# Performance work log

Measured on AMD Instinct MI355X. Metric: run time of the kernel, lower is better.

The kernel has to match this reference:

```python
import jax, jax.numpy as jnp
import numpy as np

T, B, F, H, O = 2048, 256, 64, 256, 1

def setup_inputs() -> dict:
    key = jax.random.key(0)
    k0, k1, k2 = jax.random.split(key, 3)
    return {
        "x": jax.random.normal(k0, (T, B, F), jnp.float32),          # (Time, Batch, Feat)
        "W0": jax.random.normal(k1, (H, F + H), jnp.float32) * 0.05,  # i2h weight (PyTorch layout)
        "b0": jnp.zeros((H,), jnp.float32),
        "Wfc": jax.random.normal(k2, (O, H), jnp.float32) * 0.05,     # fc1 weight
        "bfc": jnp.zeros((O,), jnp.float32),
        "feature_n": 0,
    }

def reference(x, W0, b0, Wfc, bfc, feature_n):
    # RnnCell: h = tanh(Linear(cat([x_t, h], 1))); then out_t = fc1(h).
    batch = x.shape[1]
    hidden = W0.shape[0]
    h0 = jnp.zeros((batch, hidden), x.dtype)

    def step(h, x_t):
        combined = jnp.concatenate([x_t, h], axis=1)          # (B, F+H)
        h_new = jnp.tanh(combined @ W0.T + b0)                # (B, H)
        out = h_new @ Wfc.T + bfc                             # (B, O)
        return h_new, out

    _, outs = jax.lax.scan(step, h0, x)                       # (T, B, O)
    # torch.stack(outputs, 1).squeeze(2) -> (B, T)
    return jnp.transpose(outs, (1, 0, 2)).squeeze(2)
```

## Files before the change

kernel.cpp:

```cpp
#include <hip/hip_runtime.h>

#define T_STEPS 2048
#define BATCH   256
#define FEAT    64
#define HID     256
#define KAUG    320
#define NW      4
#define NTHR    256
#define XTILE   16

typedef _Float16 half8 __attribute__((ext_vector_type(8)));
typedef _Float16 half4 __attribute__((ext_vector_type(4)));
typedef float    f32x4 __attribute__((ext_vector_type(4)));
typedef float    f32x8 __attribute__((ext_vector_type(8)));

__device__ __forceinline__ float fast_tanh(float z) {
    float e = __expf(2.0f * z);
    return 1.0f - 2.0f * __builtin_amdgcn_rcpf(e + 1.0f);
}

__global__
__attribute__((amdgpu_flat_work_group_size(NTHR, NTHR), amdgpu_waves_per_eu(1, 1)))
void rnn_kernel(const float* __restrict__ x,
                const float* __restrict__ W0,
                const float* __restrict__ b0,
                const float* __restrict__ Wfc,
                const float* __restrict__ bfc,
                float* __restrict__ out)
{
    const int b    = blockIdx.x;
    const int tid  = threadIdx.x;
    const int w    = tid >> 6;
    const int lane = tid & 63;
    const int l15  = lane & 15;
    const int kg   = lane >> 4;
    const bool alane = (l15 == 0);

    __shared__ __align__(16) _Float16 h_buf[2][HID];
    __shared__ __align__(16) _Float16 x_tile[2][XTILE][FEAT];
    __shared__ __align__(16) float    out_part[NW][T_STEPS];

    half8 bw[4][10];
#pragma unroll
    for (int j = 0; j < 4; ++j) {
        const int n = (4 * w + j) * 16 + l15;
        const float* wp = W0 + n * KAUG + kg * 8;
#pragma unroll
        for (int c = 0; c < 10; ++c) {
            const f32x8 v = *reinterpret_cast<const f32x8*>(wp + c * 32);
            bw[j][c] = __builtin_convertvector(v, half8);
        }
    }

    float b0e[4] = {}, wfe[4] = {};
    if (lane < 16) {
#pragma unroll
        for (int j = 0; j < 4; ++j) {
            b0e[j] = b0[(4 * w + j) * 16 + lane];
            wfe[j] = Wfc[(4 * w + j) * 16 + lane];
        }
    }

    if (tid < HID) { h_buf[0][tid] = (_Float16)0.f; h_buf[1][tid] = (_Float16)0.f; }
    {
        const int tr = tid >> 4, f4 = (tid & 15) * 4;
        const f32x4 v = *reinterpret_cast<const f32x4*>(
            x + (size_t)tr * (BATCH * FEAT) + b * FEAT + f4);
        const half4 hv = {(_Float16)v.x, (_Float16)v.y, (_Float16)v.z, (_Float16)v.w};
        *reinterpret_cast<half4*>(&x_tile[0][tr][f4]) = hv;
    }
    __syncthreads();

    half8 af[10];
#pragma unroll
    for (int c = 0; c < 10; ++c) af[c] = half8{};

    float p_prev = 0.f;
    const f32x4 zero4 = {0.f, 0.f, 0.f, 0.f};

    for (int t = 0; t < T_STEPS; ++t) {
        const int cur = t & 1;
        const int nxt = cur ^ 1;
        const int xb  = (t >> 4) & 1;

        const bool do_stage = ((t & 15) == 0) && (t + XTILE < T_STEPS);
        const int tr = tid >> 4, f4 = (tid & 15) * 4;
        f32x4 xld = zero4;
        if (do_stage) {
            xld = *reinterpret_cast<const f32x4*>(
                x + (size_t)(t + XTILE + tr) * (BATCH * FEAT) + b * FEAT + f4);
        }

        if (alane) {
            af[0] = *reinterpret_cast<const half8*>(&x_tile[xb][t & 15][kg * 8]);
            af[1] = *reinterpret_cast<const half8*>(&x_tile[xb][t & 15][32 + kg * 8]);
#pragma unroll
            for (int c = 2; c < 10; ++c)
                af[c] = *reinterpret_cast<const half8*>(&h_buf[cur][(c - 2) * 32 + kg * 8]);
        }

        {
            float p = p_prev;
            p += __shfl_xor(p, 1, 64);
            p += __shfl_xor(p, 2, 64);
            p += __shfl_xor(p, 4, 64);
            p += __shfl_xor(p, 8, 64);
            if (lane == 0) out_part[w][(t + T_STEPS - 1) & (T_STEPS - 1)] = p;
        }

        f32x4 aE[4], aO[4];
#pragma unroll
        for (int j = 0; j < 4; ++j) {
            aE[j] = __builtin_amdgcn_mfma_f32_16x16x32_f16(af[0], bw[j][0], zero4, 0, 0, 0);
            aO[j] = __builtin_amdgcn_mfma_f32_16x16x32_f16(af[1], bw[j][1], zero4, 0, 0, 0);
        }
#pragma unroll
        for (int c = 2; c < 10; c += 2) {
#pragma unroll
            for (int j = 0; j < 4; ++j) {
                aE[j] = __builtin_amdgcn_mfma_f32_16x16x32_f16(af[c],     bw[j][c],     aE[j], 0, 0, 0);
                aO[j] = __builtin_amdgcn_mfma_f32_16x16x32_f16(af[c + 1], bw[j][c + 1], aO[j], 0, 0, 0);
            }
        }

        if (do_stage) {
            const half4 hv = {(_Float16)xld.x, (_Float16)xld.y,
                              (_Float16)xld.z, (_Float16)xld.w};
            *reinterpret_cast<half4*>(&x_tile[xb ^ 1][tr][f4]) = hv;
        }

        float pnew = 0.f;
        if (lane < 16) {
#pragma unroll
            for (int j = 0; j < 4; ++j) {
                const float z = aE[j][0] + aO[j][0] + b0e[j];
                const float h = fast_tanh(z);
                pnew = fmaf(wfe[j], h, pnew);
                h_buf[nxt][(4 * w + j) * 16 + lane] = (_Float16)h;
            }
        }
        p_prev = pnew;

        __syncthreads();
    }

    {
        float p = p_prev;
        p += __shfl_xor(p, 1, 64);
        p += __shfl_xor(p, 2, 64);
        p += __shfl_xor(p, 4, 64);
        p += __shfl_xor(p, 8, 64);
        if (lane == 0) out_part[w][T_STEPS - 1] = p;
    }
    __syncthreads();

    const float bfc_r = bfc[0];
#pragma unroll
    for (int i = 0; i < 2; ++i) {
        const int t0 = tid * 8 + i * 4;
        f32x4 s = {bfc_r, bfc_r, bfc_r, bfc_r};
#pragma unroll
        for (int ww = 0; ww < NW; ++ww)
            s += *reinterpret_cast<const f32x4*>(&out_part[ww][t0]);
        *reinterpret_cast<f32x4*>(out + b * T_STEPS + t0) = s;
    }
}

extern "C" void kernel_launch(void* const* d_in, const int* in_sizes, int n_in,
                              void* d_out, int out_size, void* d_ws, size_t ws_size,
                              hipStream_t stream) {
    const float* x   = (const float*)d_in[0];
    const float* W0  = (const float*)d_in[1];
    const float* b0  = (const float*)d_in[2];
    const float* Wfc = (const float*)d_in[3];
    const float* bfc = (const float*)d_in[4];
    float* out = (float*)d_out;

    rnn_kernel<<<dim3(BATCH), dim3(NTHR), 0, stream>>>(x, W0, b0, Wfc, bfc, out);
}
```

Baseline: 1.727 ms.

## Split hidden units across 16 waves per block with LDS atomic output reduction

Each block grows from 4 to 16 waves, and each wave now owns one 16-column slice of the hidden state instead of four. The per-wave serial MFMA chain per timestep becomes 10 instructions instead of 40. The per-wave output partial buffers are replaced by a single LDS buffer updated with atomicAdd. X staging becomes a 4-deep ring prefetched two tiles ahead. In exchange, the per-step barrier must synchronize 1024 threads, and 16 LDS atomics per step contend on a single address.

```diff
diff --git a/kernel.cpp b/kernel.cpp
--- a/kernel.cpp
+++ b/kernel.cpp
@@ -5,12 +5,13 @@
 #define FEAT    64
 #define HID     256
 #define KAUG    320
-#define NW      4
-#define NTHR    256
+#define NW      16
+#define NTHR    1024
 #define XTILE   16
+#define NXB     4
+#define NTILES  (T_STEPS / XTILE)
 
 typedef _Float16 half8 __attribute__((ext_vector_type(8)));
-typedef _Float16 half4 __attribute__((ext_vector_type(4)));
 typedef float    f32x4 __attribute__((ext_vector_type(4)));
 typedef float    f32x8 __attribute__((ext_vector_type(8)));
 
@@ -20,7 +21,7 @@
 }
 
 __global__
-__attribute__((amdgpu_flat_work_group_size(NTHR, NTHR), amdgpu_waves_per_eu(1, 1)))
+__attribute__((amdgpu_flat_work_group_size(NTHR, NTHR), amdgpu_waves_per_eu(4, 4)))
 void rnn_kernel(const float* __restrict__ x,
                 const float* __restrict__ W0,
                 const float* __restrict__ b0,
@@ -37,38 +38,38 @@
     const bool alane = (l15 == 0);
 
     __shared__ __align__(16) _Float16 h_buf[2][HID];
-    __shared__ __align__(16) _Float16 x_tile[2][XTILE][FEAT];
-    __shared__ __align__(16) float    out_part[NW][T_STEPS];
+    __shared__ __align__(16) _Float16 x_tile[NXB][XTILE][FEAT];
+    __shared__ __align__(16) float    out_buf[T_STEPS];
 
-    half8 bw[4][10];
-#pragma unroll
-    for (int j = 0; j < 4; ++j) {
-        const int n = (4 * w + j) * 16 + l15;
-        const float* wp = W0 + n * KAUG + kg * 8;
+    half8 bw[10];
+    {
+        const float* wp = W0 + (16 * w + l15) * KAUG + kg * 8;
 #pragma unroll
         for (int c = 0; c < 10; ++c) {
             const f32x8 v = *reinterpret_cast<const f32x8*>(wp + c * 32);
-            bw[j][c] = __builtin_convertvector(v, half8);
+            bw[c] = __builtin_convertvector(v, half8);
         }
     }
 
-    float b0e[4] = {}, wfe[4] = {};
+    float b0e = 0.f, wfe = 0.f;
     if (lane < 16) {
-#pragma unroll
-        for (int j = 0; j < 4; ++j) {
-            b0e[j] = b0[(4 * w + j) * 16 + lane];
-            wfe[j] = Wfc[(4 * w + j) * 16 + lane];
-        }
+        b0e = b0[16 * w + lane];
+        wfe = Wfc[16 * w + lane];
     }
+    const float bfc_r = bfc[0];
 
     if (tid < HID) { h_buf[0][tid] = (_Float16)0.f; h_buf[1][tid] = (_Float16)0.f; }
-    {
-        const int tr = tid >> 4, f4 = (tid & 15) * 4;
-        const f32x4 v = *reinterpret_cast<const f32x4*>(
-            x + (size_t)tr * (BATCH * FEAT) + b * FEAT + f4);
-        const half4 hv = {(_Float16)v.x, (_Float16)v.y, (_Float16)v.z, (_Float16)v.w};
-        *reinterpret_cast<half4*>(&x_tile[0][tr][f4]) = hv;
+    out_buf[tid]        = bfc_r;
+    out_buf[tid + NTHR] = bfc_r;
+
+    const int tr = tid >> 6;
+    const int fx = tid & 63;
+#pragma unroll
+    for (int ti = 0; ti < 2; ++ti) {
+        const float v = x[(size_t)(XTILE * ti + tr) * (BATCH * FEAT) + b * FEAT + fx];
+        x_tile[ti][tr][fx] = (_Float16)v;
     }
+    float xhold = x[(size_t)(XTILE * 2 + tr) * (BATCH * FEAT) + b * FEAT + fx];
     __syncthreads();
 
     half8 af[10];
@@ -81,22 +82,16 @@
     for (int t = 0; t < T_STEPS; ++t) {
         const int cur = t & 1;
         const int nxt = cur ^ 1;
-        const int xb  = (t >> 4) & 1;
-
-        const bool do_stage = ((t & 15) == 0) && (t + XTILE < T_STEPS);
-        const int tr = tid >> 4, f4 = (tid & 15) * 4;
-        f32x4 xld = zero4;
-        if (do_stage) {
-            xld = *reinterpret_cast<const f32x4*>(
-                x + (size_t)(t + XTILE + tr) * (BATCH * FEAT) + b * FEAT + f4);
-        }
+        const int xb  = (t >> 4) & (NXB - 1);
 
         if (alane) {
-            af[0] = *reinterpret_cast<const half8*>(&x_tile[xb][t & 15][kg * 8]);
-            af[1] = *reinterpret_cast<const half8*>(&x_tile[xb][t & 15][32 + kg * 8]);
+            const _Float16* xr = &x_tile[xb][t & 15][kg * 8];
+            af[0] = *reinterpret_cast<const half8*>(xr);
+            af[1] = *reinterpret_cast<const half8*>(xr + 32);
+            const _Float16* hr = &h_buf[cur][kg * 8];
 #pragma unroll
             for (int c = 2; c < 10; ++c)
-                af[c] = *reinterpret_cast<const half8*>(&h_buf[cur][(c - 2) * 32 + kg * 8]);
+                af[c] = *reinterpret_cast<const half8*>(hr + (c - 2) * 32);
         }
 
         {
@@ -105,39 +100,30 @@
             p += __shfl_xor(p, 2, 64);
             p += __shfl_xor(p, 4, 64);
             p += __shfl_xor(p, 8, 64);
-            if (lane == 0) out_part[w][(t + T_STEPS - 1) & (T_STEPS - 1)] = p;
+            if (lane == 0 && t > 0) atomicAdd(&out_buf[t - 1], p);
         }
 
-        f32x4 aE[4], aO[4];
-#pragma unroll
-        for (int j = 0; j < 4; ++j) {
-            aE[j] = __builtin_amdgcn_mfma_f32_16x16x32_f16(af[0], bw[j][0], zero4, 0, 0, 0);
-            aO[j] = __builtin_amdgcn_mfma_f32_16x16x32_f16(af[1], bw[j][1], zero4, 0, 0, 0);
-        }
+        f32x4 a0 = __builtin_amdgcn_mfma_f32_16x16x32_f16(af[0], bw[0], zero4, 0, 0, 0);
+        f32x4 a1 = __builtin_amdgcn_mfma_f32_16x16x32_f16(af[1], bw[1], zero4, 0, 0, 0);
 #pragma unroll
         for (int c = 2; c < 10; c += 2) {
-#pragma unroll
-            for (int j = 0; j < 4; ++j) {
-                aE[j] = __builtin_amdgcn_mfma_f32_16x16x32_f16(af[c],     bw[j][c],     aE[j], 0, 0, 0);
-                aO[j] = __builtin_amdgcn_mfma_f32_16x16x32_f16(af[c + 1], bw[j][c + 1], aO[j], 0, 0, 0);
-            }
+            a0 = __builtin_amdgcn_mfma_f32_16x16x32_f16(af[c],     bw[c],     a0, 0, 0, 0);
+            a1 = __builtin_amdgcn_mfma_f32_16x16x32_f16(af[c + 1], bw[c + 1], a1, 0, 0, 0);
         }
 
-        if (do_stage) {
-            const half4 hv = {(_Float16)xld.x, (_Float16)xld.y,
-                              (_Float16)xld.z, (_Float16)xld.w};
-            *reinterpret_cast<half4*>(&x_tile[xb ^ 1][tr][f4]) = hv;
+        if ((t & 15) == 0) {
+            const int ti = t >> 4;
+            if (ti + 2 < NTILES)
+                x_tile[(ti + 2) & (NXB - 1)][tr][fx] = (_Float16)xhold;
+            if (ti + 3 < NTILES)
+                xhold = x[(size_t)(XTILE * (ti + 3) + tr) * (BATCH * FEAT) + b * FEAT + fx];
         }
 
         float pnew = 0.f;
         if (lane < 16) {
-#pragma unroll
-            for (int j = 0; j < 4; ++j) {
-                const float z = aE[j][0] + aO[j][0] + b0e[j];
-                const float h = fast_tanh(z);
-                pnew = fmaf(wfe[j], h, pnew);
-                h_buf[nxt][(4 * w + j) * 16 + lane] = (_Float16)h;
-            }
+            const float h = fast_tanh(a0[0] + a1[0] + b0e);
+            h_buf[nxt][16 * w + lane] = (_Float16)h;
+            pnew = wfe * h;
         }
         p_prev = pnew;
 
@@ -150,20 +136,12 @@
         p += __shfl_xor(p, 2, 64);
         p += __shfl_xor(p, 4, 64);
         p += __shfl_xor(p, 8, 64);
-        if (lane == 0) out_part[w][T_STEPS - 1] = p;
+        if (lane == 0) atomicAdd(&out_buf[T_STEPS - 1], p);
     }
     __syncthreads();
 
-    const float bfc_r = bfc[0];
-#pragma unroll
-    for (int i = 0; i < 2; ++i) {
-        const int t0 = tid * 8 + i * 4;
-        f32x4 s = {bfc_r, bfc_r, bfc_r, bfc_r};
-#pragma unroll
-        for (int ww = 0; ww < NW; ++ww)
-            s += *reinterpret_cast<const f32x4*>(&out_part[ww][t0]);
-        *reinterpret_cast<f32x4*>(out + b * T_STEPS + t0) = s;
-    }
+    out[b * T_STEPS + tid]        = out_buf[tid];
+    out[b * T_STEPS + tid + NTHR] = out_buf[tid + NTHR];
 }
 
 extern "C" void kernel_launch(void* const* d_in, const int* in_sizes, int n_in,
```

Result: slower. 1.834 ms (+6.2%).
